# Kernel optimization log

Hardware: AMD Instinct MI355X
Metric: run time of the kernel (lower is better)

The kernel has to match this reference:

```python
import jax, jax.numpy as jnp
import numpy as np

BATCH, FEAT = 128, 1024
CLS = 500
HID = 512

def setup_inputs() -> dict:
    key = jax.random.key(0)
    ks = jax.random.split(key, 6)
    return {
        "image_feats": jax.random.normal(ks[0], (BATCH, FEAT), dtype=jnp.float32),
        "attributes": jax.random.normal(ks[1], (CLS, FEAT), dtype=jnp.float32),
        "W1": jax.random.normal(ks[2], (HID, 2 * FEAT), dtype=jnp.float32) * 0.02,
        "b1": jax.random.normal(ks[3], (HID,), dtype=jnp.float32) * 0.02,
        "W2": jax.random.normal(ks[4], (1, HID), dtype=jnp.float32) * 0.02,
        "b2": jax.random.normal(ks[5], (1,), dtype=jnp.float32) * 0.02,
    }

def reference(image_feats, attributes, W1, b1, W2, b2):
    feat_dim = image_feats.shape[1]
    # fc1 on cat([img, attr]) == img @ W1[:, :F].T + attr @ W1[:, F:].T + b1
    # computed via broadcast-add, never materializing the (B, C, 2F) concat.
    img_part = image_feats @ W1[:, :feat_dim].T          # (B, HID)
    attr_part = attributes @ W1[:, feat_dim:].T          # (C, HID)
    h = jax.nn.relu(img_part[:, None, :] + attr_part[None, :, :] + b1)  # (B, C, HID)
    out = jax.nn.sigmoid(jnp.einsum('bch,oh->bco', h, W2) + b2)          # (B, C, 1)
    return out[..., 0]  # (B, C)
```

## Files before the change

kernel.cpp:

```cpp
#include <hip/hip_runtime.h>
#include <math.h>

#define BATCH 128
#define FEAT  1024
#define CLS   500
#define HID   512
#define ISPL  8
#define ASPL  6

constexpr int BM = 64, BN = 64, BK = 16;
constexpr int TB = 16, TC = 16, HC = 256;

constexpr int NIMG  = BATCH * HID;
constexpr int NATTR = CLS * HID;

__global__ __launch_bounds__(256) void gemm_bt_splitk(
    const float* __restrict__ img, const float* __restrict__ attr,
    const float* __restrict__ W1,
    float* __restrict__ imgP, float* __restrict__ attrP)
{
    __shared__ float As[BK][BM + 4];
    __shared__ float Bs[BK][BN + 4];

    const int t   = threadIdx.x;
    const int bid = blockIdx.x;

    const float* A;
    float* P;
    int M, boff, m0, n0, kt0, nkt;
    if (bid < 128) {
        const int z   = bid >> 4;
        const int rem = bid & 15;
        A = img; P = imgP + (size_t)z * NIMG;
        M = BATCH; boff = 0;
        m0 = (rem >> 3) * BM;
        n0 = (rem & 7) * BN;
        kt0 = z * 8;  nkt = 8;
    } else {
        const int a   = bid - 128;
        const int z   = a / 64;
        const int rem = a & 63;
        A = attr; P = attrP + (size_t)z * NATTR;
        M = CLS; boff = FEAT;
        m0 = (rem >> 3) * BM;
        n0 = (rem & 7) * BN;
        kt0 = (z < 4) ? z * 11 : 44 + (z - 4) * 10;
        nkt = (z < 4) ? 11 : 10;
    }

    const int K   = FEAT;
    const int ldb = 2 * FEAT;

    const int lrow = t >> 2;
    const int lk   = (t & 3) * 4;

    const int tn = t & 15;
    const int tm = t >> 4;

    float acc[4][4];
    #pragma unroll
    for (int i = 0; i < 4; ++i)
        #pragma unroll
        for (int j = 0; j < 4; ++j) acc[i][j] = 0.f;

    for (int kt = 0; kt < nkt; ++kt) {
        const int kk = (kt0 + kt) * BK;
        {
            const int m = m0 + lrow;
            float4 av = make_float4(0.f, 0.f, 0.f, 0.f);
            if (m < M)
                av = *(const float4*)&A[(size_t)m * K + kk + lk];
            As[lk + 0][lrow] = av.x;
            As[lk + 1][lrow] = av.y;
            As[lk + 2][lrow] = av.z;
            As[lk + 3][lrow] = av.w;

            const int n = n0 + lrow;
            const float4 bv =
                *(const float4*)&W1[(size_t)n * ldb + boff + kk + lk];
            Bs[lk + 0][lrow] = bv.x;
            Bs[lk + 1][lrow] = bv.y;
            Bs[lk + 2][lrow] = bv.z;
            Bs[lk + 3][lrow] = bv.w;
        }
        __syncthreads();
        #pragma unroll
        for (int k = 0; k < BK; ++k) {
            const float4 a = *(const float4*)&As[k][tm * 4];
            const float4 b = *(const float4*)&Bs[k][tn * 4];
            acc[0][0] = fmaf(a.x, b.x, acc[0][0]);
            acc[0][1] = fmaf(a.x, b.y, acc[0][1]);
            acc[0][2] = fmaf(a.x, b.z, acc[0][2]);
            acc[0][3] = fmaf(a.x, b.w, acc[0][3]);
            acc[1][0] = fmaf(a.y, b.x, acc[1][0]);
            acc[1][1] = fmaf(a.y, b.y, acc[1][1]);
            acc[1][2] = fmaf(a.y, b.z, acc[1][2]);
            acc[1][3] = fmaf(a.y, b.w, acc[1][3]);
            acc[2][0] = fmaf(a.z, b.x, acc[2][0]);
            acc[2][1] = fmaf(a.z, b.y, acc[2][1]);
            acc[2][2] = fmaf(a.z, b.z, acc[2][2]);
            acc[2][3] = fmaf(a.z, b.w, acc[2][3]);
            acc[3][0] = fmaf(a.w, b.x, acc[3][0]);
            acc[3][1] = fmaf(a.w, b.y, acc[3][1]);
            acc[3][2] = fmaf(a.w, b.z, acc[3][2]);
            acc[3][3] = fmaf(a.w, b.w, acc[3][3]);
        }
        __syncthreads();
    }

    #pragma unroll
    for (int i = 0; i < 4; ++i) {
        const int m = m0 + tm * 4 + i;
        if (m < M) {
            float4 v = make_float4(acc[i][0], acc[i][1], acc[i][2], acc[i][3]);
            *(float4*)&P[(size_t)m * HID + n0 + tn * 4] = v;
        }
    }
}

__global__ __launch_bounds__(256) void merge_kernel(
    const float* __restrict__ imgP, const float* __restrict__ attrP,
    const float* __restrict__ b1,
    float* __restrict__ imgF, float* __restrict__ attrF)
{
    const int g = blockIdx.x * 256 + threadIdx.x;
    const float4* imgP4  = (const float4*)imgP;
    const float4* attrP4 = (const float4*)attrP;
    const float4* b14    = (const float4*)b1;
    if (g < NIMG / 4) {
        float4 s = imgP4[g];
        #pragma unroll
        for (int zz = 1; zz < ISPL; ++zz) {
            const float4 p = imgP4[zz * (NIMG / 4) + g];
            s.x += p.x; s.y += p.y; s.z += p.z; s.w += p.w;
        }
        const float4 bb = b14[g & (HID / 4 - 1)];
        s.x += bb.x; s.y += bb.y; s.z += bb.z; s.w += bb.w;
        ((float4*)imgF)[g] = s;
    } else if (g < NIMG / 4 + NATTR / 4) {
        const int j = g - NIMG / 4;
        float4 s = attrP4[j];
        #pragma unroll
        for (int zz = 1; zz < ASPL; ++zz) {
            const float4 p = attrP4[zz * (NATTR / 4) + j];
            s.x += p.x; s.y += p.y; s.z += p.z; s.w += p.w;
        }
        ((float4*)attrF)[j] = s;
    }
}

__global__ __launch_bounds__(256) void pair_kernel(
    const float* __restrict__ imgF, const float* __restrict__ attrF,
    const float* __restrict__ W2, const float* __restrict__ b2,
    float* __restrict__ out)
{
    __shared__ float U[TB][HC + 4];
    __shared__ float V[TC][HC + 4];
    __shared__ float w2s[HID];

    const int t  = threadIdx.x;
    const int c0 = blockIdx.x * TC;
    const int b0 = blockIdx.y * TB;

    w2s[t]       = W2[t];
    w2s[t + 256] = W2[t + 256];

    const int ci = t & 15;
    const int bi = t >> 4;

    float acc = 0.f;
    for (int hc = 0; hc < HID; hc += HC) {
        __syncthreads();
        #pragma unroll
        for (int rep = 0; rep < 4; ++rep) {
            const int e   = rep * 256 + t;
            const int row = e >> 6;
            const int c4  = (e & 63) * 4;
            *(float4*)&U[row][c4] =
                *(const float4*)&imgF[(b0 + row) * HID + hc + c4];
            const int c = c0 + row;
            float4 v = make_float4(0.f, 0.f, 0.f, 0.f);
            if (c < CLS)
                v = *(const float4*)&attrF[c * HID + hc + c4];
            *(float4*)&V[row][c4] = v;
        }
        __syncthreads();
        #pragma unroll
        for (int h4 = 0; h4 < HC / 4; ++h4) {
            const float4 u = *(const float4*)&U[bi][h4 * 4];
            const float4 v = *(const float4*)&V[ci][h4 * 4];
            const float4 w = *(const float4*)&w2s[hc + h4 * 4];
            acc = fmaf(fmaxf(u.x + v.x, 0.f), w.x, acc);
            acc = fmaf(fmaxf(u.y + v.y, 0.f), w.y, acc);
            acc = fmaf(fmaxf(u.z + v.z, 0.f), w.z, acc);
            acc = fmaf(fmaxf(u.w + v.w, 0.f), w.w, acc);
        }
    }

    const int b = b0 + bi;
    const int c = c0 + ci;
    if (c < CLS) {
        const float x = acc + b2[0];
        out[b * CLS + c] = 1.f / (1.f + __expf(-x));
    }
}

extern "C" void kernel_launch(void* const* d_in, const int* in_sizes, int n_in,
                              void* d_out, int out_size, void* d_ws, size_t ws_size,
                              hipStream_t stream) {
    const float* img  = (const float*)d_in[0];
    const float* attr = (const float*)d_in[1];
    const float* W1   = (const float*)d_in[2];
    const float* b1   = (const float*)d_in[3];
    const float* W2   = (const float*)d_in[4];
    const float* b2   = (const float*)d_in[5];
    float* out = (float*)d_out;

    float* ws    = (float*)d_ws;
    float* imgP  = ws;
    float* attrP = imgP  + (size_t)ISPL * NIMG;
    float* imgF  = attrP + (size_t)ASPL * NATTR;
    float* attrF = imgF  + (size_t)NIMG;

    gemm_bt_splitk<<<dim3(512), 256, 0, stream>>>(img, attr, W1, imgP, attrP);

    const int n4 = NIMG / 4 + NATTR / 4;
    merge_kernel<<<(n4 + 255) / 256, 256, 0, stream>>>(imgP, attrP, b1, imgF, attrF);

    dim3 pgrid((CLS + TC - 1) / TC, BATCH / TB);
    pair_kernel<<<pgrid, 256, 0, stream>>>(imgF, attrF, W2, b2, out);
}
```

Baseline: 95.90 us.

## Double-buffer split-K GEMM tiles and load full hidden dim in pair kernel

The split-K GEMM now keeps two shared-memory buffers and issues the global loads for the next K tile before computing the current one, writing them into the other buffer afterward. This cuts one barrier per iteration and hides global load latency behind the FMAs. The pair kernel now loads the whole 512-wide hidden dimension for U and V in one pass, removing the hc loop and its extra barriers. That doubles shared memory use per block, which may lower occupancy.

```diff
diff --git a/kernel.cpp b/kernel.cpp
--- a/kernel.cpp
+++ b/kernel.cpp
@@ -9,7 +9,7 @@
 #define ASPL  6
 
 constexpr int BM = 64, BN = 64, BK = 16;
-constexpr int TB = 16, TC = 16, HC = 256;
+constexpr int TB = 16, TC = 16;
 
 constexpr int NIMG  = BATCH * HID;
 constexpr int NATTR = CLS * HID;
@@ -19,8 +19,8 @@
     const float* __restrict__ W1,
     float* __restrict__ imgP, float* __restrict__ attrP)
 {
-    __shared__ float As[BK][BM + 4];
-    __shared__ float Bs[BK][BN + 4];
+    __shared__ float As[2][BK][BM + 4];
+    __shared__ float Bs[2][BK][BN + 4];
 
     const int t   = threadIdx.x;
     const int bid = blockIdx.x;
@@ -53,9 +53,24 @@
 
     const int lrow = t >> 2;
     const int lk   = (t & 3) * 4;
-
-    const int tn = t & 15;
-    const int tm = t >> 4;
+    const int tn   = t & 15;
+    const int tm   = t >> 4;
+
+    const int mrow = m0 + lrow;
+    const bool mok = (mrow < M);
+    const float* Aptr = A  + (size_t)mrow * K + lk;
+    const float* Bptr = W1 + (size_t)(n0 + lrow) * ldb + boff + lk;
+
+    {
+        const int kk = kt0 * BK;
+        float4 av = make_float4(0.f, 0.f, 0.f, 0.f);
+        if (mok) av = *(const float4*)&Aptr[kk];
+        const float4 bv = *(const float4*)&Bptr[kk];
+        As[0][lk + 0][lrow] = av.x; As[0][lk + 1][lrow] = av.y;
+        As[0][lk + 2][lrow] = av.z; As[0][lk + 3][lrow] = av.w;
+        Bs[0][lk + 0][lrow] = bv.x; Bs[0][lk + 1][lrow] = bv.y;
+        Bs[0][lk + 2][lrow] = bv.z; Bs[0][lk + 3][lrow] = bv.w;
+    }
 
     float acc[4][4];
     #pragma unroll
@@ -64,30 +79,21 @@
         for (int j = 0; j < 4; ++j) acc[i][j] = 0.f;
 
     for (int kt = 0; kt < nkt; ++kt) {
-        const int kk = (kt0 + kt) * BK;
-        {
-            const int m = m0 + lrow;
-            float4 av = make_float4(0.f, 0.f, 0.f, 0.f);
-            if (m < M)
-                av = *(const float4*)&A[(size_t)m * K + kk + lk];
-            As[lk + 0][lrow] = av.x;
-            As[lk + 1][lrow] = av.y;
-            As[lk + 2][lrow] = av.z;
-            As[lk + 3][lrow] = av.w;
-
-            const int n = n0 + lrow;
-            const float4 bv =
-                *(const float4*)&W1[(size_t)n * ldb + boff + kk + lk];
-            Bs[lk + 0][lrow] = bv.x;
-            Bs[lk + 1][lrow] = bv.y;
-            Bs[lk + 2][lrow] = bv.z;
-            Bs[lk + 3][lrow] = bv.w;
-        }
         __syncthreads();
+        const int cur  = kt & 1;
+        const bool more = (kt + 1 < nkt);
+
+        float4 av = make_float4(0.f, 0.f, 0.f, 0.f), bv;
+        if (more) {
+            const int kk = (kt0 + kt + 1) * BK;
+            if (mok) av = *(const float4*)&Aptr[kk];
+            bv = *(const float4*)&Bptr[kk];
+        }
+
         #pragma unroll
         for (int k = 0; k < BK; ++k) {
-            const float4 a = *(const float4*)&As[k][tm * 4];
-            const float4 b = *(const float4*)&Bs[k][tn * 4];
+            const float4 a = *(const float4*)&As[cur][k][tm * 4];
+            const float4 b = *(const float4*)&Bs[cur][k][tn * 4];
             acc[0][0] = fmaf(a.x, b.x, acc[0][0]);
             acc[0][1] = fmaf(a.x, b.y, acc[0][1]);
             acc[0][2] = fmaf(a.x, b.z, acc[0][2]);
@@ -105,7 +111,14 @@
             acc[3][2] = fmaf(a.w, b.z, acc[3][2]);
             acc[3][3] = fmaf(a.w, b.w, acc[3][3]);
         }
-        __syncthreads();
+
+        if (more) {
+            const int nxt = cur ^ 1;
+            As[nxt][lk + 0][lrow] = av.x; As[nxt][lk + 1][lrow] = av.y;
+            As[nxt][lk + 2][lrow] = av.z; As[nxt][lk + 3][lrow] = av.w;
+            Bs[nxt][lk + 0][lrow] = bv.x; Bs[nxt][lk + 1][lrow] = bv.y;
+            Bs[nxt][lk + 2][lrow] = bv.z; Bs[nxt][lk + 3][lrow] = bv.w;
+        }
     }
 
     #pragma unroll
@@ -154,8 +167,8 @@
     const float* __restrict__ W2, const float* __restrict__ b2,
     float* __restrict__ out)
 {
-    __shared__ float U[TB][HC + 4];
-    __shared__ float V[TC][HC + 4];
+    __shared__ float U[TB][HID + 4];
+    __shared__ float V[TC][HID + 4];
     __shared__ float w2s[HID];
 
     const int t  = threadIdx.x;
@@ -165,36 +178,34 @@
     w2s[t]       = W2[t];
     w2s[t + 256] = W2[t + 256];
 
+    #pragma unroll
+    for (int rep = 0; rep < 8; ++rep) {
+        const int e   = rep * 256 + t;
+        const int row = e >> 7;
+        const int c4  = (e & 127) * 4;
+        *(float4*)&U[row][c4] =
+            *(const float4*)&imgF[(b0 + row) * HID + c4];
+        const int c = c0 + row;
+        float4 v = make_float4(0.f, 0.f, 0.f, 0.f);
+        if (c < CLS)
+            v = *(const float4*)&attrF[c * HID + c4];
+        *(float4*)&V[row][c4] = v;
+    }
+    __syncthreads();
+
     const int ci = t & 15;
     const int bi = t >> 4;
 
     float acc = 0.f;
-    for (int hc = 0; hc < HID; hc += HC) {
-        __syncthreads();
-        #pragma unroll
-        for (int rep = 0; rep < 4; ++rep) {
-            const int e   = rep * 256 + t;
-            const int row = e >> 6;
-            const int c4  = (e & 63) * 4;
-            *(float4*)&U[row][c4] =
-                *(const float4*)&imgF[(b0 + row) * HID + hc + c4];
-            const int c = c0 + row;
-            float4 v = make_float4(0.f, 0.f, 0.f, 0.f);
-            if (c < CLS)
-                v = *(const float4*)&attrF[c * HID + hc + c4];
-            *(float4*)&V[row][c4] = v;
-        }
-        __syncthreads();
-        #pragma unroll
-        for (int h4 = 0; h4 < HC / 4; ++h4) {
-            const float4 u = *(const float4*)&U[bi][h4 * 4];
-            const float4 v = *(const float4*)&V[ci][h4 * 4];
-            const float4 w = *(const float4*)&w2s[hc + h4 * 4];
-            acc = fmaf(fmaxf(u.x + v.x, 0.f), w.x, acc);
-            acc = fmaf(fmaxf(u.y + v.y, 0.f), w.y, acc);
-            acc = fmaf(fmaxf(u.z + v.z, 0.f), w.z, acc);
-            acc = fmaf(fmaxf(u.w + v.w, 0.f), w.w, acc);
-        }
+    #pragma unroll 16
+    for (int h4 = 0; h4 < HID / 4; ++h4) {
+        const float4 u = *(const float4*)&U[bi][h4 * 4];
+        const float4 v = *(const float4*)&V[ci][h4 * 4];
+        const float4 w = *(const float4*)&w2s[h4 * 4];
+        acc = fmaf(fmaxf(u.x + v.x, 0.f), w.x, acc);
+        acc = fmaf(fmaxf(u.y + v.y, 0.f), w.y, acc);
+        acc = fmaf(fmaxf(u.z + v.z, 0.f), w.z, acc);
+        acc = fmaf(fmaxf(u.w + v.w, 0.f), w.w, acc);
     }
 
     const int b = b0 + bi;
```

Result: faster. 93.95 us, median of 2 (-2.0%).
